# Kernel optimization log

Measured on AMD Instinct MI355X. Metric: run time of the kernel, lower is better.

The kernel has to match this reference:

```python
import jax, jax.numpy as jnp
import numpy as np

LN_EPS = 1e-5


def setup_inputs() -> dict:
    key = jax.random.key(0)
    ks = jax.random.split(key, 6)
    n_nodes, mem_dim = 500000, 256
    n_upd, msg_dim = 65536, 512
    return {
        "unique_node_ids": jnp.arange(n_upd, dtype=jnp.int64) if jax.config.jax_enable_x64 else jnp.arange(n_upd, dtype=jnp.int32),
        "unique_messages": jax.random.normal(ks[0], (n_upd, msg_dim), dtype=jnp.float32),
        "timestamps": jax.random.uniform(ks[1], (n_upd,), dtype=jnp.float32),
        "memory": jax.random.normal(ks[2], (n_nodes, mem_dim), dtype=jnp.float32),
        "last_update": jnp.zeros((n_nodes,), dtype=jnp.float32),
        "W_ih": jax.random.normal(ks[3], (3 * mem_dim, msg_dim), dtype=jnp.float32) * (1.0 / np.sqrt(msg_dim)),
        "W_hh": jax.random.normal(ks[4], (3 * mem_dim, mem_dim), dtype=jnp.float32) * (1.0 / np.sqrt(mem_dim)),
        "b_ih": jnp.zeros((3 * mem_dim,), dtype=jnp.float32),
        "b_hh": jnp.zeros((3 * mem_dim,), dtype=jnp.float32),
        "ln_gamma": jnp.ones((mem_dim,), dtype=jnp.float32),
        "ln_beta": jnp.zeros((mem_dim,), dtype=jnp.float32),
    }


def _gru_cell(x, h, W_ih, W_hh, b_ih, b_hh):
    # torch.nn.GRUCell math
    gi = x @ W_ih.T + b_ih          # [N, 3H]
    gh = h @ W_hh.T + b_hh          # [N, 3H]
    i_r, i_z, i_n = jnp.split(gi, 3, axis=-1)
    h_r, h_z, h_n = jnp.split(gh, 3, axis=-1)
    r = jax.nn.sigmoid(i_r + h_r)
    z = jax.nn.sigmoid(i_z + h_z)
    n = jnp.tanh(i_n + r * h_n)
    return (1.0 - z) * n + z * h


def _layer_norm(x, gamma, beta):
    mu = jnp.mean(x, axis=-1, keepdims=True)
    var = jnp.mean(jnp.square(x - mu), axis=-1, keepdims=True)
    return (x - mu) * jax.lax.rsqrt(var + LN_EPS) * gamma + beta


def reference(unique_node_ids, unique_messages, timestamps, memory, last_update,
              W_ih, W_hh, b_ih, b_hh, ln_gamma, ln_beta):
    # gather memory rows for the nodes being updated
    h = memory[unique_node_ids]                      # [N, H]
    new_h = _gru_cell(unique_messages, h, W_ih, W_hh, b_ih, b_hh)
    new_h = _layer_norm(new_h, ln_gamma, ln_beta)
    # scatter updated rows back (get_updated_memory semantics: pure copy)
    updated_memory = memory.at[unique_node_ids].set(new_h)
    updated_last_update = last_update.at[unique_node_ids].set(timestamps)
    return updated_memory, updated_last_update
```

## Files before the change

kernel.cpp:

```cpp
#include <hip/hip_runtime.h>
#include <hip/hip_bf16.h>

typedef float  f32x4 __attribute__((ext_vector_type(4)));
typedef short  s16x8 __attribute__((ext_vector_type(8)));

#define MEMH   256
#define MSGD   512
#define G3     768
#define W_IH_ELEMS (G3*MSGD)
#define W_HH_ELEMS (G3*MEMH)
#define W_TOT_ELEMS (W_IH_ELEMS + W_HH_ELEMS)
#define W_BYTES    ((size_t)W_TOT_ELEMS * 2)

#define BM      32
#define NTHR    1024
#define AM_OFF  0
#define AH_OFF  32768
#define B_OFF   49152
#define PART_OFF 147456
#define LDS_BYTES 151552

typedef const __attribute__((address_space(1))) void* gas_p;
typedef __attribute__((address_space(3)))       void* las_p;

static __device__ __forceinline__ short f2bf(float x) {
    __hip_bfloat16 b = __float2bfloat16(x);
    return __builtin_bit_cast(short, b);
}
static __device__ __forceinline__ float bf2f(short s) {
    unsigned int u = ((unsigned int)(unsigned short)s) << 16;
    return __builtin_bit_cast(float, u);
}
static __device__ __forceinline__ s16x8 cvt8(f32x4 a, f32x4 b) {
    s16x8 s;
    s[0]=f2bf(a[0]); s[1]=f2bf(a[1]); s[2]=f2bf(a[2]); s[3]=f2bf(a[3]);
    s[4]=f2bf(b[0]); s[5]=f2bf(b[1]); s[6]=f2bf(b[2]); s[7]=f2bf(b[3]);
    return s;
}
static __device__ __forceinline__ float sigf(float x) {
    return 1.f / (1.f + __expf(-x));
}
static __device__ __forceinline__ float tanh_fast(float x) {
    float e = __expf(-2.f * fabsf(x));
    float t = (1.f - e) / (1.f + e);
    return copysignf(t, x);
}
static __device__ __forceinline__ f32x4 ntload4(const float* p) {
    return __builtin_nontemporal_load((const f32x4*)p);
}
static __device__ __forceinline__ void ntstore4(float* p, f32x4 v) {
    __builtin_nontemporal_store(v, (f32x4*)p);
}

__global__ void smu_copy_kernel(const float* __restrict__ mem,
                                const float* __restrict__ lu,
                                float* __restrict__ out_mem,
                                float* __restrict__ out_lu,
                                long n_mem4, long n_lu4) {
    long i = (long)blockIdx.x * blockDim.x + threadIdx.x;
    long stride = (long)gridDim.x * blockDim.x;
    long total = n_mem4 + n_lu4;
    for (; i < total; i += stride) {
        if (i < n_mem4) ntstore4(out_mem + i * 4, ntload4(mem + i * 4));
        else {
            long j = (i - n_mem4) * 4;
            ntstore4(out_lu + j, ntload4(lu + j));
        }
    }
}

__global__ __launch_bounds__(256)
void smu_copy_skip_kernel(const float* __restrict__ mem,
                          const float* __restrict__ lu,
                          const unsigned* __restrict__ bm,
                          float* __restrict__ out_mem,
                          float* __restrict__ out_lu,
                          long n_nodes) {
    const long nu = n_nodes * (MEMH / 4);
    const long stride = (long)gridDim.x * blockDim.x;
    const long i0 = (long)blockIdx.x * blockDim.x + threadIdx.x;

    for (long i = i0; i < nu; i += stride) {
        long r = i >> 6;
        if (!((bm[r >> 5] >> (r & 31)) & 1u))
            ntstore4(out_mem + i * 4, ntload4(mem + i * 4));
    }
    for (long i = i0; i < n_nodes; i += stride) {
        if (!((bm[i >> 5] >> (i & 31)) & 1u)) {
            float v = __builtin_nontemporal_load(lu + i);
            __builtin_nontemporal_store(v, out_lu + i);
        }
    }
}

__global__ void smu_cvtw_kernel(const float* __restrict__ wih,
                                const float* __restrict__ whh,
                                short* __restrict__ o) {
    int i = blockIdx.x * blockDim.x + threadIdx.x;
    if (i >= W_TOT_ELEMS) return;
    if (i < W_IH_ELEMS) {
        int f = i >> 9, r = i & 511, l = r >> 3, e = r & 7;
        int t = f >> 4, k = f & 15;
        int row = t * 16 + (l & 15), col = k * 32 + (l >> 4) * 8 + e;
        o[i] = f2bf(wih[row * MSGD + col]);
    } else {
        int j = i - W_IH_ELEMS;
        int f = j >> 9, r = j & 511, l = r >> 3, e = r & 7;
        int t = f >> 3, k = f & 7;
        int row = t * 16 + (l & 15), col = k * 32 + (l >> 4) * 8 + e;
        o[i] = f2bf(whh[row * MEMH + col]);
    }
}

__global__ void smu_clear_kernel(unsigned* __restrict__ p, int n) {
    int i = blockIdx.x * blockDim.x + threadIdx.x;
    if (i < n) p[i] = 0u;
}
__global__ void smu_bits_kernel(const int* __restrict__ ids,
                                unsigned* __restrict__ bm, int n) {
    int i = blockIdx.x * blockDim.x + threadIdx.x;
    if (i < n) {
        int id = ids[i];
        atomicOr(&bm[id >> 5], 1u << (id & 31));
    }
}

__global__ __launch_bounds__(NTHR, 1)
void smu_gru_dma_kernel(const int*   __restrict__ ids,
                        const float* __restrict__ msg,
                        const float* __restrict__ ts,
                        const float* __restrict__ memory,
                        const float* __restrict__ b_ih,
                        const float* __restrict__ b_hh,
                        const float* __restrict__ gamma,
                        const float* __restrict__ beta,
                        const short* __restrict__ wsw,
                        float* __restrict__ out_mem,
                        float* __restrict__ out_lu) {
    __shared__ __align__(16) unsigned char lds[LDS_BYTES];
    const int tid = threadIdx.x;
    const long base = (long)blockIdx.x * BM;

    const int lane = tid & 63;
    const int w    = tid >> 6;
    const int lr   = lane & 15;
    const int lq   = lane >> 4;
    const int lk8  = lq * 8;
    const int sw   = (lr & 7) << 4;
    const short* Wi = wsw;
    const short* Wh = wsw + W_IH_ELEMS;

    {
        const float* src = msg + base * MSGD;
        #pragma unroll
        for (int it = 0; it < 2; ++it) {
            int u = tid + NTHR * it;
            int row = u >> 6;
            f32x4 a = ntload4(src + u * 8);
            f32x4 b = ntload4(src + u * 8 + 4);
            int byte = AM_OFF + ((u * 16) ^ ((row & 7) << 4));
            *(s16x8*)(lds + byte) = cvt8(a, b);
        }
        {
            int u = tid;
            int row = u >> 5;
            int c8  = u & 31;
            int id  = ids[base + row];
            const float* hs = memory + (size_t)id * MEMH + c8 * 8;
            f32x4 a = ntload4(hs);
            f32x4 b = ntload4(hs + 4);
            int byte = AH_OFF + ((u * 16) ^ ((row & 7) << 4));
            *(s16x8*)(lds + byte) = cvt8(a, b);
        }
    }
    __syncthreads();

    const int bbase = B_OFF + w * 6144;
    f32x4 rz[2][2] = {};
    f32x4 gin[2]   = {};
    f32x4 ghn[2]   = {};

    {
        #pragma unroll
        for (int g = 0; g < 3; ++g)
            __builtin_amdgcn_global_load_lds(
                (gas_p)(const void*)(Wi + (((16 * g + w) * 16 + 0) << 9) + lane * 8),
                (las_p)(void*)(lds + bbase + g * 1024), 16, 0, 0);
        #pragma unroll
        for (int k = 0; k < 16; ++k) {
            if (k < 15) {
                const int nb = bbase + ((k + 1) & 1) * 3072;
                #pragma unroll
                for (int g = 0; g < 3; ++g)
                    __builtin_amdgcn_global_load_lds(
                        (gas_p)(const void*)(Wi + (((16 * g + w) * 16 + (k + 1)) << 9) + lane * 8),
                        (las_p)(void*)(lds + nb + g * 1024), 16, 0, 0);
                asm volatile("s_waitcnt vmcnt(3)" ::: "memory");
            } else {
                asm volatile("s_waitcnt vmcnt(0)" ::: "memory");
            }
            const int bufo = bbase + (k & 1) * 3072;
            s16x8 b0 = *(const s16x8*)(lds + bufo + 0 * 1024 + lane * 16);
            s16x8 b1 = *(const s16x8*)(lds + bufo + 1 * 1024 + lane * 16);
            s16x8 b2 = *(const s16x8*)(lds + bufo + 2 * 1024 + lane * 16);
            const int cb = (k * 32 + lk8) * 2;
            #pragma unroll
            for (int m = 0; m < 2; ++m) {
                s16x8 a = *(const s16x8*)(lds + AM_OFF + (((m*16 + lr) * 1024 + cb) ^ sw));
                rz[m][0] = __builtin_amdgcn_mfma_f32_16x16x32_bf16(a, b0, rz[m][0], 0, 0, 0);
                rz[m][1] = __builtin_amdgcn_mfma_f32_16x16x32_bf16(a, b1, rz[m][1], 0, 0, 0);
                gin[m]   = __builtin_amdgcn_mfma_f32_16x16x32_bf16(a, b2, gin[m],   0, 0, 0);
            }
        }
    }
    {
        #pragma unroll
        for (int g = 0; g < 3; ++g)
            __builtin_amdgcn_global_load_lds(
                (gas_p)(const void*)(Wh + (((16 * g + w) * 8 + 0) << 9) + lane * 8),
                (las_p)(void*)(lds + bbase + g * 1024), 16, 0, 0);
        #pragma unroll
        for (int k = 0; k < 8; ++k) {
            if (k < 7) {
                const int nb = bbase + ((k + 1) & 1) * 3072;
                #pragma unroll
                for (int g = 0; g < 3; ++g)
                    __builtin_amdgcn_global_load_lds(
                        (gas_p)(const void*)(Wh + (((16 * g + w) * 8 + (k + 1)) << 9) + lane * 8),
                        (las_p)(void*)(lds + nb + g * 1024), 16, 0, 0);
                asm volatile("s_waitcnt vmcnt(3)" ::: "memory");
            } else {
                asm volatile("s_waitcnt vmcnt(0)" ::: "memory");
            }
            const int bufo = bbase + (k & 1) * 3072;
            s16x8 b0 = *(const s16x8*)(lds + bufo + 0 * 1024 + lane * 16);
            s16x8 b1 = *(const s16x8*)(lds + bufo + 1 * 1024 + lane * 16);
            s16x8 b2 = *(const s16x8*)(lds + bufo + 2 * 1024 + lane * 16);
            const int cb = (k * 32 + lk8) * 2;
            #pragma unroll
            for (int m = 0; m < 2; ++m) {
                s16x8 a = *(const s16x8*)(lds + AH_OFF + (((m*16 + lr) * 512 + cb) ^ sw));
                rz[m][0] = __builtin_amdgcn_mfma_f32_16x16x32_bf16(a, b0, rz[m][0], 0, 0, 0);
                rz[m][1] = __builtin_amdgcn_mfma_f32_16x16x32_bf16(a, b1, rz[m][1], 0, 0, 0);
                ghn[m]   = __builtin_amdgcn_mfma_f32_16x16x32_bf16(a, b2, ghn[m],   0, 0, 0);
            }
        }
    }

    const int j = w * 16 + lr;
    f32x4 o_[2];
    {
        const float br = b_ih[j]       + b_hh[j];
        const float bz = b_ih[256 + j] + b_hh[256 + j];
        const float bihn = b_ih[512 + j], bhhn = b_hh[512 + j];
        #pragma unroll
        for (int m = 0; m < 2; ++m) {
            #pragma unroll
            for (int q = 0; q < 4; ++q) {
                int row = m * 16 + lq * 4 + q;
                float r = sigf(rz[m][0][q] + br);
                float z = sigf(rz[m][1][q] + bz);
                float n = tanh_fast(gin[m][q] + bihn + r * (ghn[m][q] + bhhn));
                float hv = bf2f(*(const short*)(lds + AH_OFF + ((row * 512 + j * 2) ^ ((row & 7) << 4))));
                o_[m][q] = (1.f - z) * n + z * hv;
            }
        }
    }

    {
        float* part = (float*)(lds + PART_OFF);
        #pragma unroll
        for (int m = 0; m < 2; ++m) {
            #pragma unroll
            for (int q = 0; q < 4; ++q) {
                float v = o_[m][q];
                float s1 = v, s2 = v * v;
                #pragma unroll
                for (int mk = 1; mk < 16; mk <<= 1) {
                    s1 += __shfl_xor(s1, mk);
                    s2 += __shfl_xor(s2, mk);
                }
                if (lr == 0) {
                    int row = m * 16 + lq * 4 + q;
                    part[(row * 16 + w) * 2]     = s1;
                    part[(row * 16 + w) * 2 + 1] = s2;
                }
            }
        }
    }
    __syncthreads();

    float mu_[2][4], inv_[2][4];
    {
        const float* part = (const float*)(lds + PART_OFF);
        #pragma unroll
        for (int m = 0; m < 2; ++m) {
            #pragma unroll
            for (int q = 0; q < 4; ++q) {
                int row = m * 16 + lq * 4 + q;
                float s1 = 0.f, s2 = 0.f;
                #pragma unroll
                for (int i = 0; i < 16; ++i) {
                    s1 += part[(row * 16 + i) * 2];
                    s2 += part[(row * 16 + i) * 2 + 1];
                }
                float mu  = s1 * (1.f / 256.f);
                float var = fmaxf(s2 * (1.f / 256.f) - mu * mu, 0.f);
                mu_[m][q]  = mu;
                inv_[m][q] = rsqrtf(var + 1e-5f);
            }
        }
    }

    {
        const float ga = gamma[j], be = beta[j];
        #pragma unroll
        for (int m = 0; m < 2; ++m) {
            #pragma unroll
            for (int q = 0; q < 4; ++q) {
                int row = m * 16 + lq * 4 + q;
                int id = ids[base + row];
                float y = (o_[m][q] - mu_[m][q]) * inv_[m][q] * ga + be;
                __builtin_nontemporal_store(y, out_mem + (size_t)id * MEMH + j);
            }
        }
        if (w == 0 && lane < 32) {
            int id = ids[base + lane];
            __builtin_nontemporal_store(ts[base + lane], out_lu + id);
        }
    }
}

__global__ __launch_bounds__(512, 4)
void smu_gru_fb_kernel(const int*   __restrict__ ids,
                       const float* __restrict__ msg,
                       const float* __restrict__ ts,
                       const float* __restrict__ memory,
                       const float* __restrict__ W_ih,
                       const float* __restrict__ W_hh,
                       const float* __restrict__ b_ih,
                       const float* __restrict__ b_hh,
                       const float* __restrict__ gamma,
                       const float* __restrict__ beta,
                       float* __restrict__ out_mem,
                       float* __restrict__ out_lu) {
    __shared__ __align__(16) unsigned char lds[51200];
    const int tid = threadIdx.x;
    const long base = (long)blockIdx.x * 32;

    {
        const float* src = msg + base * MSGD;
        #pragma unroll
        for (int it = 0; it < 4; ++it) {
            int u = tid + 512 * it;
            int row = u >> 6;
            f32x4 a = ntload4(src + u * 8);
            f32x4 b = ntload4(src + u * 8 + 4);
            int byte = ((u * 16) ^ ((row & 7) << 4));
            *(s16x8*)(lds + byte) = cvt8(a, b);
        }
        #pragma unroll
        for (int it = 0; it < 2; ++it) {
            int u = tid + 512 * it;
            int row = u >> 5;
            int c8  = u & 31;
            int id  = ids[base + row];
            const float* hs = memory + (size_t)id * MEMH + c8 * 8;
            f32x4 a = ntload4(hs);
            f32x4 b = ntload4(hs + 4);
            int byte = 32768 + ((u * 16) ^ ((row & 7) << 4));
            *(s16x8*)(lds + byte) = cvt8(a, b);
        }
    }
    __syncthreads();

    const int lane = tid & 63;
    const int w    = tid >> 6;
    const int lr   = lane & 15;
    const int lq   = lane >> 4;
    const int lk8  = lq * 8;
    const int sw   = (lr & 7) << 4;

    auto loadb = [&](const float* Wf, int t, int k, int ldk) {
        int row = t * 16 + lr;
        int col = k * 32 + lk8;
        f32x4 x = *(const f32x4*)(Wf + (size_t)row * ldk + col);
        f32x4 y = *(const f32x4*)(Wf + (size_t)row * ldk + col + 4);
        return cvt8(x, y);
    };

    f32x4 rz[2][2][2] = {};
    f32x4 gin[2][2]   = {};
    f32x4 ghn[2][2]   = {};

    for (int k = 0; k < 16; ++k) {
        const int cb = (k * 32 + lk8) * 2;
        #pragma unroll
        for (int m = 0; m < 2; ++m) {
            s16x8 a = *(const s16x8*)(lds + (((m*16 + lr) * 1024 + cb) ^ sw));
            #pragma unroll
            for (int ci = 0; ci < 2; ++ci) {
                s16x8 b0 = loadb(W_ih, w + 8*ci + 0,  k, MSGD);
                s16x8 b1 = loadb(W_ih, w + 8*ci + 16, k, MSGD);
                s16x8 b2 = loadb(W_ih, w + 8*ci + 32, k, MSGD);
                rz[m][ci][0] = __builtin_amdgcn_mfma_f32_16x16x32_bf16(a, b0, rz[m][ci][0], 0, 0, 0);
                rz[m][ci][1] = __builtin_amdgcn_mfma_f32_16x16x32_bf16(a, b1, rz[m][ci][1], 0, 0, 0);
                gin[m][ci]   = __builtin_amdgcn_mfma_f32_16x16x32_bf16(a, b2, gin[m][ci],   0, 0, 0);
            }
        }
    }
    for (int k = 0; k < 8; ++k) {
        const int cb = (k * 32 + lk8) * 2;
        #pragma unroll
        for (int m = 0; m < 2; ++m) {
            s16x8 a = *(const s16x8*)(lds + 32768 + (((m*16 + lr) * 512 + cb) ^ sw));
            #pragma unroll
            for (int ci = 0; ci < 2; ++ci) {
                s16x8 b0 = loadb(W_hh, w + 8*ci + 0,  k, MEMH);
                s16x8 b1 = loadb(W_hh, w + 8*ci + 16, k, MEMH);
                s16x8 b2 = loadb(W_hh, w + 8*ci + 32, k, MEMH);
                rz[m][ci][0] = __builtin_amdgcn_mfma_f32_16x16x32_bf16(a, b0, rz[m][ci][0], 0, 0, 0);
                rz[m][ci][1] = __builtin_amdgcn_mfma_f32_16x16x32_bf16(a, b1, rz[m][ci][1], 0, 0, 0);
                ghn[m][ci]   = __builtin_amdgcn_mfma_f32_16x16x32_bf16(a, b2, ghn[m][ci],   0, 0, 0);
            }
        }
    }

    f32x4 o_[2][2];
    #pragma unroll
    for (int ci = 0; ci < 2; ++ci) {
        const int j = (w + 8*ci) * 16 + lr;
        const float br = b_ih[j]       + b_hh[j];
        const float bz = b_ih[256 + j] + b_hh[256 + j];
        const float bihn = b_ih[512 + j], bhhn = b_hh[512 + j];
        #pragma unroll
        for (int m = 0; m < 2; ++m) {
            #pragma unroll
            for (int q = 0; q < 4; ++q) {
                int row = m * 16 + lq * 4 + q;
                float r = sigf(rz[m][ci][0][q] + br);
                float z = sigf(rz[m][ci][1][q] + bz);
                float n = tanh_fast(gin[m][ci][q] + bihn + r * (ghn[m][ci][q] + bhhn));
                float hv = bf2f(*(const short*)(lds + 32768 + ((row * 512 + j * 2) ^ ((row & 7) << 4))));
                o_[m][ci][q] = (1.f - z) * n + z * hv;
            }
        }
    }

    float* part = (float*)(lds + 49152);
    #pragma unroll
    for (int m = 0; m < 2; ++m)
        #pragma unroll
        for (int q = 0; q < 4; ++q) {
            float v0 = o_[m][0][q], v1 = o_[m][1][q];
            float s1 = v0 + v1, s2 = v0*v0 + v1*v1;
            #pragma unroll
            for (int mk = 1; mk < 16; mk <<= 1) {
                s1 += __shfl_xor(s1, mk);
                s2 += __shfl_xor(s2, mk);
            }
            if (lr == 0) {
                int row = m * 16 + lq * 4 + q;
                part[(row * 8 + w) * 2]     = s1;
                part[(row * 8 + w) * 2 + 1] = s2;
            }
        }
    __syncthreads();

    #pragma unroll
    for (int ci = 0; ci < 2; ++ci) {
        const int j = (w + 8*ci) * 16 + lr;
        const float ga = gamma[j], be = beta[j];
        #pragma unroll
        for (int m = 0; m < 2; ++m)
            #pragma unroll
            for (int q = 0; q < 4; ++q) {
                int row = m * 16 + lq * 4 + q;
                float s1 = 0.f, s2 = 0.f;
                #pragma unroll
                for (int i = 0; i < 8; ++i) {
                    s1 += part[(row * 8 + i) * 2];
                    s2 += part[(row * 8 + i) * 2 + 1];
                }
                float mu  = s1 * (1.f / 256.f);
                float var = fmaxf(s2 * (1.f / 256.f) - mu * mu, 0.f);
                float inv = rsqrtf(var + 1e-5f);
                int id = ids[base + row];
                float y = (o_[m][ci][q] - mu) * inv * ga + be;
                __builtin_nontemporal_store(y, out_mem + (size_t)id * MEMH + j);
            }
    }
    if (w == 0 && lane < 32) {
        int id = ids[base + lane];
        __builtin_nontemporal_store(ts[base + lane], out_lu + id);
    }
}

extern "C" void kernel_launch(void* const* d_in, const int* in_sizes, int n_in,
                              void* d_out, int out_size, void* d_ws, size_t ws_size,
                              hipStream_t stream) {
    (void)n_in; (void)out_size;
    const int*   ids = (const int*)  d_in[0];
    const float* msg = (const float*)d_in[1];
    const float* ts  = (const float*)d_in[2];
    const float* mem = (const float*)d_in[3];
    const float* lu  = (const float*)d_in[4];
    const float* Wih = (const float*)d_in[5];
    const float* Whh = (const float*)d_in[6];
    const float* bih = (const float*)d_in[7];
    const float* bhh = (const float*)d_in[8];
    const float* gam = (const float*)d_in[9];
    const float* bet = (const float*)d_in[10];

    const int  n_upd   = in_sizes[0];
    const long n_nodes = (long)in_sizes[3] / MEMH;

    float* out_mem = (float*)d_out;
    float* out_lu  = out_mem + (size_t)n_nodes * MEMH;

    const int    bm_words     = (int)((n_nodes + 31) / 32) + 4;
    const size_t bm_bytes_pad = (size_t)bm_words * 4;
    const bool ws_ok = (d_ws != nullptr) && (ws_size >= W_BYTES + bm_bytes_pad);

    short*    wsw = (short*)d_ws;
    unsigned* bm  = (unsigned*)((char*)d_ws + W_BYTES);

    if (ws_ok) {
        smu_clear_kernel<<<(bm_words + 255) / 256, 256, 0, stream>>>(bm, bm_words);
        smu_bits_kernel<<<(n_upd + 255) / 256, 256, 0, stream>>>(ids, bm, n_upd);
        smu_copy_skip_kernel<<<2048, 256, 0, stream>>>(mem, lu, bm, out_mem, out_lu, n_nodes);
        smu_cvtw_kernel<<<(W_TOT_ELEMS + 255) / 256, 256, 0, stream>>>(Wih, Whh, wsw);
        smu_gru_dma_kernel<<<n_upd / BM, NTHR, 0, stream>>>(
            ids, msg, ts, mem, bih, bhh, gam, bet, wsw, out_mem, out_lu);
    } else {
        long n_mem4 = n_nodes * (MEMH / 4);
        long n_lu4  = n_nodes / 4;
        smu_copy_kernel<<<2048, 256, 0, stream>>>(mem, lu, out_mem, out_lu, n_mem4, n_lu4);
        smu_gru_fb_kernel<<<n_upd / 32, 512, 0, stream>>>(
            ids, msg, ts, mem, Wih, Whh, bih, bhh, gam, bet, out_mem, out_lu);
    }
}
```

Baseline: 371.4 us.

## Fuse skip-copy into GRU kernel via interleaved blocks and share weight tiles

Merges the bitmap-masked memory copy into the GRU kernel: odd blocks copy the untouched memory rows with 4-way unrolled loads, and even blocks run the GRU, so the bandwidth-bound copy overlaps the matmul work. The GRU tile grows from 32 to 64 rows. The weight layout is reordered so the whole workgroup cooperatively loads one shared 48-tile K-slice per step, rather than each wave streaming its own double-buffered weights, which cuts redundant weight traffic per row. LayerNorm stats are reduced with shuffles. The cost is more block-wide barriers per K step, single-buffered weight loads with a full vmcnt(0) wait, and copy blocks that hold large LDS allocations and so compete with GRU blocks for occupancy.

```diff
diff --git a/kernel.cpp b/kernel.cpp
--- a/kernel.cpp
+++ b/kernel.cpp
@@ -12,13 +12,14 @@
 #define W_TOT_ELEMS (W_IH_ELEMS + W_HH_ELEMS)
 #define W_BYTES    ((size_t)W_TOT_ELEMS * 2)
 
-#define BM      32
-#define NTHR    1024
-#define AM_OFF  0
-#define AH_OFF  32768
-#define B_OFF   49152
+#define BM     64
+#define NTHR   1024
+#define WB_OFF   0
+#define AM_OFF   49152
+#define AH_OFF   114688
 #define PART_OFF 147456
-#define LDS_BYTES 151552
+#define STAT_OFF 155648
+#define LDS_BYTES 156160
 
 typedef const __attribute__((address_space(1))) void* gas_p;
 typedef __attribute__((address_space(3)))       void* las_p;
@@ -69,30 +70,6 @@
     }
 }
 
-__global__ __launch_bounds__(256)
-void smu_copy_skip_kernel(const float* __restrict__ mem,
-                          const float* __restrict__ lu,
-                          const unsigned* __restrict__ bm,
-                          float* __restrict__ out_mem,
-                          float* __restrict__ out_lu,
-                          long n_nodes) {
-    const long nu = n_nodes * (MEMH / 4);
-    const long stride = (long)gridDim.x * blockDim.x;
-    const long i0 = (long)blockIdx.x * blockDim.x + threadIdx.x;
-
-    for (long i = i0; i < nu; i += stride) {
-        long r = i >> 6;
-        if (!((bm[r >> 5] >> (r & 31)) & 1u))
-            ntstore4(out_mem + i * 4, ntload4(mem + i * 4));
-    }
-    for (long i = i0; i < n_nodes; i += stride) {
-        if (!((bm[i >> 5] >> (i & 31)) & 1u)) {
-            float v = __builtin_nontemporal_load(lu + i);
-            __builtin_nontemporal_store(v, out_lu + i);
-        }
-    }
-}
-
 __global__ void smu_cvtw_kernel(const float* __restrict__ wih,
                                 const float* __restrict__ whh,
                                 short* __restrict__ o) {
@@ -100,13 +77,13 @@
     if (i >= W_TOT_ELEMS) return;
     if (i < W_IH_ELEMS) {
         int f = i >> 9, r = i & 511, l = r >> 3, e = r & 7;
-        int t = f >> 4, k = f & 15;
+        int k = f / 48, t = f - k * 48;
         int row = t * 16 + (l & 15), col = k * 32 + (l >> 4) * 8 + e;
         o[i] = f2bf(wih[row * MSGD + col]);
     } else {
         int j = i - W_IH_ELEMS;
         int f = j >> 9, r = j & 511, l = r >> 3, e = r & 7;
-        int t = f >> 3, k = f & 7;
+        int k = f / 48, t = f - k * 48;
         int row = t * 16 + (l & 15), col = k * 32 + (l >> 4) * 8 + e;
         o[i] = f2bf(whh[row * MEMH + col]);
     }
@@ -126,20 +103,95 @@
 }
 
 __global__ __launch_bounds__(NTHR, 1)
-void smu_gru_dma_kernel(const int*   __restrict__ ids,
-                        const float* __restrict__ msg,
-                        const float* __restrict__ ts,
-                        const float* __restrict__ memory,
-                        const float* __restrict__ b_ih,
-                        const float* __restrict__ b_hh,
-                        const float* __restrict__ gamma,
-                        const float* __restrict__ beta,
-                        const short* __restrict__ wsw,
-                        float* __restrict__ out_mem,
-                        float* __restrict__ out_lu) {
+void smu_fused_kernel(const int*   __restrict__ ids,
+                      const float* __restrict__ msg,
+                      const float* __restrict__ ts,
+                      const float* __restrict__ memory,
+                      const float* __restrict__ lu,
+                      const float* __restrict__ b_ih,
+                      const float* __restrict__ b_hh,
+                      const float* __restrict__ gamma,
+                      const float* __restrict__ beta,
+                      const short* __restrict__ wsw,
+                      const unsigned* __restrict__ bm,
+                      float* __restrict__ out_mem,
+                      float* __restrict__ out_lu,
+                      long n_nodes) {
     __shared__ __align__(16) unsigned char lds[LDS_BYTES];
     const int tid = threadIdx.x;
-    const long base = (long)blockIdx.x * BM;
+    const int bid = blockIdx.x;
+
+    if (bid & 1) {
+        const long nblk   = gridDim.x >> 1;
+        const long cid    = bid >> 1;
+        const long nu     = n_nodes * (MEMH / 4);
+        const long stride = nblk * NTHR;
+        const long i0     = cid * NTHR + tid;
+
+        for (long i = i0; i < nu; i += stride * 4) {
+            long  u0 = i, u1 = i + stride, u2 = i + stride * 2, u3 = i + stride * 3;
+            f32x4 v0, v1, v2, v3;
+            bool  f0 = false, f1 = false, f2 = false, f3 = false;
+            {
+                long r0 = u0 >> 6;
+                f0 = !((bm[r0 >> 5] >> (r0 & 31)) & 1u);
+                if (f0) v0 = ntload4(memory + u0 * 4);
+            }
+            if (u1 < nu) {
+                long r1 = u1 >> 6;
+                f1 = !((bm[r1 >> 5] >> (r1 & 31)) & 1u);
+                if (f1) v1 = ntload4(memory + u1 * 4);
+            }
+            if (u2 < nu) {
+                long r2 = u2 >> 6;
+                f2 = !((bm[r2 >> 5] >> (r2 & 31)) & 1u);
+                if (f2) v2 = ntload4(memory + u2 * 4);
+            }
+            if (u3 < nu) {
+                long r3 = u3 >> 6;
+                f3 = !((bm[r3 >> 5] >> (r3 & 31)) & 1u);
+                if (f3) v3 = ntload4(memory + u3 * 4);
+            }
+            if (f0) ntstore4(out_mem + u0 * 4, v0);
+            if (f1) ntstore4(out_mem + u1 * 4, v1);
+            if (f2) ntstore4(out_mem + u2 * 4, v2);
+            if (f3) ntstore4(out_mem + u3 * 4, v3);
+        }
+        for (long i = i0; i < n_nodes; i += stride) {
+            if (!((bm[i >> 5] >> (i & 31)) & 1u)) {
+                float v = __builtin_nontemporal_load(lu + i);
+                __builtin_nontemporal_store(v, out_lu + i);
+            }
+        }
+        return;
+    }
+
+    const long base = (long)(bid >> 1) * BM;
+
+    {
+        const float* src = msg + base * MSGD;
+        #pragma unroll
+        for (int it = 0; it < 4; ++it) {
+            int u = tid + NTHR * it;
+            int row = u >> 6;
+            f32x4 a = ntload4(src + u * 8);
+            f32x4 b = ntload4(src + u * 8 + 4);
+            int byte = AM_OFF + ((u * 16) ^ ((row & 7) << 4));
+            *(s16x8*)(lds + byte) = cvt8(a, b);
+        }
+        #pragma unroll
+        for (int it = 0; it < 2; ++it) {
+            int u = tid + NTHR * it;
+            int row = u >> 5;
+            int c8  = u & 31;
+            int id  = ids[base + row];
+            const float* hs = memory + (size_t)id * MEMH + c8 * 8;
+            f32x4 a = ntload4(hs);
+            f32x4 b = ntload4(hs + 4);
+            int byte = AH_OFF + ((u * 16) ^ ((row & 7) << 4));
+            *(s16x8*)(lds + byte) = cvt8(a, b);
+        }
+    }
 
     const int lane = tid & 63;
     const int w    = tid >> 6;
@@ -150,117 +202,90 @@
     const short* Wi = wsw;
     const short* Wh = wsw + W_IH_ELEMS;
 
-    {
-        const float* src = msg + base * MSGD;
-        #pragma unroll
-        for (int it = 0; it < 2; ++it) {
-            int u = tid + NTHR * it;
-            int row = u >> 6;
-            f32x4 a = ntload4(src + u * 8);
-            f32x4 b = ntload4(src + u * 8 + 4);
-            int byte = AM_OFF + ((u * 16) ^ ((row & 7) << 4));
-            *(s16x8*)(lds + byte) = cvt8(a, b);
-        }
-        {
-            int u = tid;
-            int row = u >> 5;
-            int c8  = u & 31;
-            int id  = ids[base + row];
-            const float* hs = memory + (size_t)id * MEMH + c8 * 8;
-            f32x4 a = ntload4(hs);
-            f32x4 b = ntload4(hs + 4);
-            int byte = AH_OFF + ((u * 16) ^ ((row & 7) << 4));
-            *(s16x8*)(lds + byte) = cvt8(a, b);
-        }
-    }
+    const int tile0 = 3 * w;
+
+    #pragma unroll
+    for (int g = 0; g < 3; ++g)
+        __builtin_amdgcn_global_load_lds(
+            (gas_p)(const void*)(Wi + ((size_t)(0 * 48 + tile0 + g) << 9) + lane * 8),
+            (las_p)(void*)(lds + WB_OFF + (tile0 + g) * 1024), 16, 0, 0);
     __syncthreads();
 
-    const int bbase = B_OFF + w * 6144;
-    f32x4 rz[2][2] = {};
-    f32x4 gin[2]   = {};
-    f32x4 ghn[2]   = {};
-
-    {
-        #pragma unroll
-        for (int g = 0; g < 3; ++g)
-            __builtin_amdgcn_global_load_lds(
-                (gas_p)(const void*)(Wi + (((16 * g + w) * 16 + 0) << 9) + lane * 8),
-                (las_p)(void*)(lds + bbase + g * 1024), 16, 0, 0);
-        #pragma unroll
-        for (int k = 0; k < 16; ++k) {
-            if (k < 15) {
-                const int nb = bbase + ((k + 1) & 1) * 3072;
-                #pragma unroll
-                for (int g = 0; g < 3; ++g)
-                    __builtin_amdgcn_global_load_lds(
-                        (gas_p)(const void*)(Wi + (((16 * g + w) * 16 + (k + 1)) << 9) + lane * 8),
-                        (las_p)(void*)(lds + nb + g * 1024), 16, 0, 0);
-                asm volatile("s_waitcnt vmcnt(3)" ::: "memory");
-            } else {
-                asm volatile("s_waitcnt vmcnt(0)" ::: "memory");
-            }
-            const int bufo = bbase + (k & 1) * 3072;
-            s16x8 b0 = *(const s16x8*)(lds + bufo + 0 * 1024 + lane * 16);
-            s16x8 b1 = *(const s16x8*)(lds + bufo + 1 * 1024 + lane * 16);
-            s16x8 b2 = *(const s16x8*)(lds + bufo + 2 * 1024 + lane * 16);
-            const int cb = (k * 32 + lk8) * 2;
-            #pragma unroll
-            for (int m = 0; m < 2; ++m) {
-                s16x8 a = *(const s16x8*)(lds + AM_OFF + (((m*16 + lr) * 1024 + cb) ^ sw));
-                rz[m][0] = __builtin_amdgcn_mfma_f32_16x16x32_bf16(a, b0, rz[m][0], 0, 0, 0);
-                rz[m][1] = __builtin_amdgcn_mfma_f32_16x16x32_bf16(a, b1, rz[m][1], 0, 0, 0);
-                gin[m]   = __builtin_amdgcn_mfma_f32_16x16x32_bf16(a, b2, gin[m],   0, 0, 0);
-            }
-        }
-    }
-    {
-        #pragma unroll
-        for (int g = 0; g < 3; ++g)
-            __builtin_amdgcn_global_load_lds(
-                (gas_p)(const void*)(Wh + (((16 * g + w) * 8 + 0) << 9) + lane * 8),
-                (las_p)(void*)(lds + bbase + g * 1024), 16, 0, 0);
-        #pragma unroll
-        for (int k = 0; k < 8; ++k) {
-            if (k < 7) {
-                const int nb = bbase + ((k + 1) & 1) * 3072;
-                #pragma unroll
-                for (int g = 0; g < 3; ++g)
-                    __builtin_amdgcn_global_load_lds(
-                        (gas_p)(const void*)(Wh + (((16 * g + w) * 8 + (k + 1)) << 9) + lane * 8),
-                        (las_p)(void*)(lds + nb + g * 1024), 16, 0, 0);
-                asm volatile("s_waitcnt vmcnt(3)" ::: "memory");
-            } else {
-                asm volatile("s_waitcnt vmcnt(0)" ::: "memory");
-            }
-            const int bufo = bbase + (k & 1) * 3072;
-            s16x8 b0 = *(const s16x8*)(lds + bufo + 0 * 1024 + lane * 16);
-            s16x8 b1 = *(const s16x8*)(lds + bufo + 1 * 1024 + lane * 16);
-            s16x8 b2 = *(const s16x8*)(lds + bufo + 2 * 1024 + lane * 16);
-            const int cb = (k * 32 + lk8) * 2;
-            #pragma unroll
-            for (int m = 0; m < 2; ++m) {
-                s16x8 a = *(const s16x8*)(lds + AH_OFF + (((m*16 + lr) * 512 + cb) ^ sw));
-                rz[m][0] = __builtin_amdgcn_mfma_f32_16x16x32_bf16(a, b0, rz[m][0], 0, 0, 0);
-                rz[m][1] = __builtin_amdgcn_mfma_f32_16x16x32_bf16(a, b1, rz[m][1], 0, 0, 0);
-                ghn[m]   = __builtin_amdgcn_mfma_f32_16x16x32_bf16(a, b2, ghn[m],   0, 0, 0);
-            }
+    f32x4 acc[4][3] = {};
+    f32x4 accn[4]   = {};
+
+    #pragma unroll
+    for (int k = 0; k < 16; ++k) {
+        s16x8 b0 = *(const s16x8*)(lds + WB_OFF + (w)      * 1024 + lane * 16);
+        s16x8 b1 = *(const s16x8*)(lds + WB_OFF + (w + 16) * 1024 + lane * 16);
+        s16x8 b2 = *(const s16x8*)(lds + WB_OFF + (w + 32) * 1024 + lane * 16);
+        __syncthreads();
+        if (k < 15) {
+            #pragma unroll
+            for (int g = 0; g < 3; ++g)
+                __builtin_amdgcn_global_load_lds(
+                    (gas_p)(const void*)(Wi + ((size_t)((k + 1) * 48 + tile0 + g) << 9) + lane * 8),
+                    (las_p)(void*)(lds + WB_OFF + (tile0 + g) * 1024), 16, 0, 0);
+        } else {
+            #pragma unroll
+            for (int g = 0; g < 3; ++g)
+                __builtin_amdgcn_global_load_lds(
+                    (gas_p)(const void*)(Wh + ((size_t)(0 * 48 + tile0 + g) << 9) + lane * 8),
+                    (las_p)(void*)(lds + WB_OFF + (tile0 + g) * 1024), 16, 0, 0);
+        }
+        const int cb = (k * 32 + lk8) * 2;
+        #pragma unroll
+        for (int m = 0; m < 4; ++m) {
+            s16x8 a = *(const s16x8*)(lds + AM_OFF + (((m*16 + lr) * 1024 + cb) ^ sw));
+            acc[m][0] = __builtin_amdgcn_mfma_f32_16x16x32_bf16(a, b0, acc[m][0], 0, 0, 0);
+            acc[m][1] = __builtin_amdgcn_mfma_f32_16x16x32_bf16(a, b1, acc[m][1], 0, 0, 0);
+            acc[m][2] = __builtin_amdgcn_mfma_f32_16x16x32_bf16(a, b2, acc[m][2], 0, 0, 0);
+        }
+        asm volatile("s_waitcnt vmcnt(0)" ::: "memory");
+        __syncthreads();
+    }
+
+    #pragma unroll
+    for (int k = 0; k < 8; ++k) {
+        s16x8 b0 = *(const s16x8*)(lds + WB_OFF + (w)      * 1024 + lane * 16);
+        s16x8 b1 = *(const s16x8*)(lds + WB_OFF + (w + 16) * 1024 + lane * 16);
+        s16x8 b2 = *(const s16x8*)(lds + WB_OFF + (w + 32) * 1024 + lane * 16);
+        __syncthreads();
+        if (k < 7) {
+            #pragma unroll
+            for (int g = 0; g < 3; ++g)
+                __builtin_amdgcn_global_load_lds(
+                    (gas_p)(const void*)(Wh + ((size_t)((k + 1) * 48 + tile0 + g) << 9) + lane * 8),
+                    (las_p)(void*)(lds + WB_OFF + (tile0 + g) * 1024), 16, 0, 0);
+        }
+        const int cb = (k * 32 + lk8) * 2;
+        #pragma unroll
+        for (int m = 0; m < 4; ++m) {
+            s16x8 a = *(const s16x8*)(lds + AH_OFF + (((m*16 + lr) * 512 + cb) ^ sw));
+            acc[m][0] = __builtin_amdgcn_mfma_f32_16x16x32_bf16(a, b0, acc[m][0], 0, 0, 0);
+            acc[m][1] = __builtin_amdgcn_mfma_f32_16x16x32_bf16(a, b1, acc[m][1], 0, 0, 0);
+            accn[m]   = __builtin_amdgcn_mfma_f32_16x16x32_bf16(a, b2, accn[m],   0, 0, 0);
+        }
+        if (k < 7) {
+            asm volatile("s_waitcnt vmcnt(0)" ::: "memory");
+            __syncthreads();
         }
     }
 
     const int j = w * 16 + lr;
-    f32x4 o_[2];
+    f32x4 o_[4];
     {
         const float br = b_ih[j]       + b_hh[j];
         const float bz = b_ih[256 + j] + b_hh[256 + j];
         const float bihn = b_ih[512 + j], bhhn = b_hh[512 + j];
         #pragma unroll
-        for (int m = 0; m < 2; ++m) {
+        for (int m = 0; m < 4; ++m) {
             #pragma unroll
             for (int q = 0; q < 4; ++q) {
                 int row = m * 16 + lq * 4 + q;
-                float r = sigf(rz[m][0][q] + br);
-                float z = sigf(rz[m][1][q] + bz);
-                float n = tanh_fast(gin[m][q] + bihn + r * (ghn[m][q] + bhhn));
+                float r = sigf(acc[m][0][q] + br);
+                float z = sigf(acc[m][1][q] + bz);
+                float n = tanh_fast(acc[m][2][q] + bihn + r * (accn[m][q] + bhhn));
                 float hv = bf2f(*(const short*)(lds + AH_OFF + ((row * 512 + j * 2) ^ ((row & 7) << 4))));
                 o_[m][q] = (1.f - z) * n + z * hv;
             }
@@ -270,7 +295,7 @@
     {
         float* part = (float*)(lds + PART_OFF);
         #pragma unroll
-        for (int m = 0; m < 2; ++m) {
+        for (int m = 0; m < 4; ++m) {
             #pragma unroll
             for (int q = 0; q < 4; ++q) {
                 float v = o_[m][q];
@@ -290,41 +315,42 @@
     }
     __syncthreads();
 
-    float mu_[2][4], inv_[2][4];
     {
         const float* part = (const float*)(lds + PART_OFF);
-        #pragma unroll
-        for (int m = 0; m < 2; ++m) {
+        int row = w * 4 + lq;
+        float s1 = part[(row * 16 + lr) * 2];
+        float s2 = part[(row * 16 + lr) * 2 + 1];
+        #pragma unroll
+        for (int mk = 1; mk < 16; mk <<= 1) {
+            s1 += __shfl_xor(s1, mk);
+            s2 += __shfl_xor(s2, mk);
+        }
+        if (lr == 0) {
+            float mu  = s1 * (1.f / 256.f);
+            float var = fmaxf(s2 * (1.f / 256.f) - mu * mu, 0.f);
+            float* st = (float*)(lds + STAT_OFF);
+            st[row * 2]     = mu;
+            st[row * 2 + 1] = rsqrtf(var + 1e-5f);
+        }
+    }
+    __syncthreads();
+
+    {
+        const float* st = (const float*)(lds + STAT_OFF);
+        const float ga = gamma[j], be = beta[j];
+        #pragma unroll
+        for (int m = 0; m < 4; ++m) {
             #pragma unroll
             for (int q = 0; q < 4; ++q) {
                 int row = m * 16 + lq * 4 + q;
-                float s1 = 0.f, s2 = 0.f;
-                #pragma unroll
-                for (int i = 0; i < 16; ++i) {
-                    s1 += part[(row * 16 + i) * 2];
-                    s2 += part[(row * 16 + i) * 2 + 1];
-                }
-                float mu  = s1 * (1.f / 256.f);
-                float var = fmaxf(s2 * (1.f / 256.f) - mu * mu, 0.f);
-                mu_[m][q]  = mu;
-                inv_[m][q] = rsqrtf(var + 1e-5f);
-            }
-        }
-    }
-
-    {
-        const float ga = gamma[j], be = beta[j];
-        #pragma unroll
-        for (int m = 0; m < 2; ++m) {
-            #pragma unroll
-            for (int q = 0; q < 4; ++q) {
-                int row = m * 16 + lq * 4 + q;
+                float mu  = st[row * 2];
+                float inv = st[row * 2 + 1];
                 int id = ids[base + row];
-                float y = (o_[m][q] - mu_[m][q]) * inv_[m][q] * ga + be;
+                float y = (o_[m][q] - mu) * inv * ga + be;
                 __builtin_nontemporal_store(y, out_mem + (size_t)id * MEMH + j);
             }
         }
-        if (w == 0 && lane < 32) {
+        if (w == 0) {
             int id = ids[base + lane];
             __builtin_nontemporal_store(ts[base + lane], out_lu + id);
         }
@@ -525,13 +551,15 @@
     short*    wsw = (short*)d_ws;
     unsigned* bm  = (unsigned*)((char*)d_ws + W_BYTES);
 
+    const int grid = n_upd / BM;
+
     if (ws_ok) {
+        smu_cvtw_kernel<<<(W_TOT_ELEMS + 255) / 256, 256, 0, stream>>>(Wih, Whh, wsw);
         smu_clear_kernel<<<(bm_words + 255) / 256, 256, 0, stream>>>(bm, bm_words);
         smu_bits_kernel<<<(n_upd + 255) / 256, 256, 0, stream>>>(ids, bm, n_upd);
-        smu_copy_skip_kernel<<<2048, 256, 0, stream>>>(mem, lu, bm, out_mem, out_lu, n_nodes);
-        smu_cvtw_kernel<<<(W_TOT_ELEMS + 255) / 256, 256, 0, stream>>>(Wih, Whh, wsw);
-        smu_gru_dma_kernel<<<n_upd / BM, NTHR, 0, stream>>>(
-            ids, msg, ts, mem, bih, bhh, gam, bet, wsw, out_mem, out_lu);
+        smu_fused_kernel<<<2 * grid, NTHR, 0, stream>>>(
+            ids, msg, ts, mem, lu, bih, bhh, gam, bet,
+            wsw, bm, out_mem, out_lu, n_nodes);
     } else {
         long n_mem4 = n_nodes * (MEMH / 4);
         long n_lu4  = n_nodes / 4;
```

Result: faster. 342.7 us (-7.7%).
